# Optimization experiments

Measured on AMD Instinct MI355X. Metric: run time of the kernel, lower is better.

## Reference

```python
import jax, jax.numpy as jnp
import numpy as np

B, C, K, F = 16, 64, 128, 6
HORIZON_S = 3.0  # conflict_horizon_s default
EPS = 1e-06


def setup_inputs() -> dict:
    rng = np.random.default_rng(0)
    # base adjacency: sparse random directed graph, zero diagonal
    A = (rng.random((B, K, K)) < 0.05).astype(np.float32)
    A[:, np.arange(K), np.arange(K)] = 0.0
    # candidates: exactly one unordered-pair edit (state in {0:none,1:i->j,2:j->i})
    cand = np.repeat(A[:, None], C, axis=1).copy()
    i = rng.integers(0, K - 1, (B, C))
    j = i + 1 + (rng.integers(0, K - 1, (B, C)) % (K - 1 - i))
    state = rng.integers(0, 3, (B, C))
    bidx = np.arange(B)[:, None] * np.ones((1, C), dtype=np.int64)
    cidx = np.ones((B, 1), dtype=np.int64) * np.arange(C)[None, :]
    cand[bidx, cidx, i, j] = (state == 1).astype(np.float32)
    cand[bidx, cidx, j, i] = (state == 2).astype(np.float32)
    cand[:, 0] = A  # candidate 0 is NOOP (keep A_t)
    # agent features: (x, y, yaw, vx, vy, pad)
    feat = rng.normal(size=(B, K, F)).astype(np.float32)
    feat[..., 0:2] *= 20.0  # spread positions over ~40m
    mask = (rng.random((B, K)) > 0.1).astype(np.float32)
    return {
        "A_t": jnp.asarray(A),
        "candidate_A": jnp.asarray(cand),
        "agent_feat": jnp.asarray(feat),
        "agent_mask": jnp.asarray(mask),
    }


def _edit_tokens(A_t, candidate_A):
    # vectorized version of EBSTM.extract_edit_tokens
    Bn, Cn, Kn, _ = candidate_A.shape
    base = A_t > 0.5                      # [B,K,K]
    cb = candidate_A > 0.5                # [B,C,K,K]
    diff = cb != base[:, None]            # [B,C,K,K]
    upper = jnp.triu(jnp.ones((Kn, Kn), dtype=bool), k=1)
    pairdiff = (diff | jnp.swapaxes(diff, -1, -2)) & upper
    flat = pairdiff.reshape(Bn, Cn, Kn * Kn)
    changed = flat.any(-1)                # [B,C]
    idx = jnp.argmax(flat, axis=-1)       # first changed pair in row-major (i,j) order
    i = idx // Kn
    j = idx % Kn
    barange = jnp.arange(Bn)[:, None]
    carange = jnp.arange(Cn)[None, :]
    b_ij = base[barange, i, j]
    b_ji = base[barange, j, i]
    c_ij = cb[barange, carange, i, j]
    c_ji = cb[barange, carange, j, i]
    prev = jnp.where(b_ij & ~b_ji, 1, jnp.where(b_ji & ~b_ij, 2, 0))
    nxt = jnp.where(c_ij & ~c_ji, 1, jnp.where(c_ji & ~c_ij, 2, 0))
    tokens = jnp.stack([i, j, prev, nxt], axis=-1).astype(jnp.int32)
    return tokens * changed[..., None].astype(jnp.int32)


def _relation_state3(cb):
    # cb: bool [B,C,K,K]
    at = jnp.swapaxes(cb, -1, -2)
    return ((cb & ~at).astype(jnp.int32) * 1
            + (~cb & at).astype(jnp.int32) * 2
            + (cb & at).astype(jnp.int32) * 3)


def _batched_acyclic(cb, agent_mask):
    # vectorized Kahn zero-indegree peel, matching EBSTM._is_acyclic semantics:
    #  - indegree counts edges from ALL sources (valid or not)
    #  - only valid nodes are ever removed
    #  - special case: <=1 valid node is acyclic
    Bn, Cn, Kn, _ = cb.shape
    valid = (agent_mask > 0.5)[:, None, :]           # [B,1,K]
    Ai = cb.astype(jnp.int32)                        # [B,C,K,K]
    indeg = Ai.sum(axis=-2) * valid.astype(jnp.int32)  # [B,C,K]
    removed = jnp.zeros((Bn, Cn, Kn), dtype=bool)

    def body(t, carry):
        indeg, removed = carry
        rem = valid & (~removed) & (indeg == 0)
        dec = jnp.einsum('bci,bcij->bcj', rem.astype(jnp.int32), Ai)
        return indeg - dec, removed | rem

    indeg, removed = jax.lax.fori_loop(0, Kn, body, (indeg, removed))
    vcount = valid.astype(jnp.int32).sum(-1)          # [B,1]
    return (removed.astype(jnp.int32).sum(-1) == vcount) | (vcount <= 1)


def _pair_dists(agent_feat):
    pos = agent_feat[..., 0:2]
    vel = agent_feat[..., 3:5]
    # _pair_distance: d[b,i,j] = |pos_i - pos_j|
    d = jnp.linalg.norm(pos[:, :, None] - pos[:, None, :], axis=-1)
    # _pair_closest_approach_distance: r[b,i,j] = pos_j - pos_i
    r = pos[:, None, :] - pos[:, :, None]
    v = vel[:, None, :] - vel[:, :, None]
    vv = (v * v).sum(-1)
    rv = (r * v).sum(-1)
    t_star = jnp.clip(-rv / (vv + EPS), 0.0, HORIZON_S)
    dmin = jnp.linalg.norm(r + v * t_star[..., None], axis=-1)
    eye = jnp.eye(dmin.shape[-1], dtype=bool)[None]
    dmin = jnp.where(eye, jnp.inf, dmin)
    return jnp.stack([d, dmin], axis=0)  # [2,B,K,K]


def reference(A_t, candidate_A, agent_feat, agent_mask):
    cb = candidate_A > 0.5
    tokens = _edit_tokens(A_t, candidate_A)          # [B,C,4] int32
    rel = _relation_state3(cb)                       # [B,C,K,K] int32
    acyclic = _batched_acyclic(cb, agent_mask)       # [B,C] bool
    dists = _pair_dists(agent_feat)                  # [2,B,K,K] float32
    return tokens, rel, acyclic, dists
```

## Files before the change

kernel.cpp:

```cpp
#include <hip/hip_runtime.h>
#include <cstdint>
#include <math.h>

#define KN 128
#define BATCH 16
#define CAND 64

typedef float vfloat4 __attribute__((ext_vector_type(4)));

static constexpr size_t TOK_OFF = 0;
static constexpr size_t REL_OFF = (size_t)BATCH * CAND * 4;
static constexpr size_t ACY_OFF = REL_OFF + (size_t)BATCH * CAND * KN * KN;
static constexpr size_t DST_OFF = ACY_OFF + (size_t)BATCH * CAND;

#define DIAG_BIG 1.0e30f

__global__ __launch_bounds__(256) void prep_kernel(const float* __restrict__ A_t,
                                                   const float* __restrict__ feat,
                                                   uint32_t* __restrict__ bits,
                                                   float* __restrict__ out) {
    int t = threadIdx.x;
    {
        int tid  = blockIdx.x * 256 + t;
        int wave = tid >> 6;
        int lane = tid & 63;
        int half = wave & 1;
        int row  = wave >> 1;
        float v = A_t[(size_t)row * KN + half * 64 + lane];
        unsigned long long m = __ballot(v > 0.5f);
        if (lane == 0) {
            bits[row * 4 + half * 2]     = (uint32_t)m;
            bits[row * 4 + half * 2 + 1] = (uint32_t)(m >> 32);
        }
    }
    {
        int bi = 2 * blockIdx.x + (t >> 7);
        int b2 = bi >> 7, i = bi & 127, j = t & 127;
        const float* fi = feat + (size_t)bi * 6;
        const float* fj = feat + (size_t)(b2 * KN + j) * 6;
        float pix = fi[0], piy = fi[1], vix = fi[3], viy = fi[4];
        float pjx = fj[0], pjy = fj[1], vjx = fj[3], vjy = fj[4];
        float dx = pix - pjx, dy = piy - pjy;
        float d = sqrtf(dx * dx + dy * dy);
        float rx = pjx - pix, ry = pjy - piy;
        float vx = vjx - vix, vy = vjy - viy;
        float vv = vx * vx + vy * vy;
        float rv = rx * vx + ry * vy;
        float ts = fminf(fmaxf(-rv / (vv + 1e-6f), 0.0f), 3.0f);
        float mx = rx + vx * ts, my = ry + vy * ts;
        float dmin = (i == j) ? DIAG_BIG : sqrtf(mx * mx + my * my);
        float* o = out + DST_OFF;
        __builtin_nontemporal_store(d,    o + (size_t)(b2 * KN + i) * KN + j);
        __builtin_nontemporal_store(dmin, o + (size_t)((BATCH + b2) * KN + i) * KN + j);
    }
}

__global__ __launch_bounds__(512, 8) void main_kernel(const float* __restrict__ cand,
                                                      const float* __restrict__ mask,
                                                      const uint32_t* __restrict__ baseBits,
                                                      float* __restrict__ out) {
    __shared__ uint32_t adj[KN][5];
    __shared__ uint32_t adjT[KN][6];
    __shared__ uint32_t baseB[KN][4];
    __shared__ uint32_t validW[4];
    __shared__ uint32_t remW[4];
    __shared__ uint32_t removedW[4];
    __shared__ int      minIdx;

    const int t    = threadIdx.x;
    const int lane = t & 63;
    const int wave = t >> 6;
    const int bc   = blockIdx.x;
    const int b    = bc >> 6;

    const float* cptr = cand + (size_t)bc * (KN * KN);

    float4 c[8];
    const int sub = lane & 31;
    #pragma unroll
    for (int m = 0; m < 8; ++m) {
        int r = (m * 8 + wave) * 2 + (lane >> 5);
        c[m] = ((const float4*)(cptr + (size_t)r * KN))[sub];
    }

    if (t == 0) minIdx = 0x7fffffff;
    if (t < 4)  removedW[t] = 0;

    baseB[t >> 2][t & 3] = baseBits[b * 512 + t];

    if (wave < 2) {
        float mv = mask[b * KN + wave * 64 + lane];
        unsigned long long m = __ballot(mv > 0.5f);
        if (lane == 0) {
            validW[wave * 2]     = (uint32_t)m;
            validW[wave * 2 + 1] = (uint32_t)(m >> 32);
        }
    }

    #pragma unroll
    for (int m = 0; m < 8; ++m) {
        int r = (m * 8 + wave) * 2 + (lane >> 5);
        const float4 v = c[m];
        uint32_t nib = (v.x > 0.5f ? 1u : 0u) | (v.y > 0.5f ? 2u : 0u) |
                       (v.z > 0.5f ? 4u : 0u) | (v.w > 0.5f ? 8u : 0u);
        uint32_t word = nib << (4 * (sub & 7));
        word |= __shfl_xor(word, 1);
        word |= __shfl_xor(word, 2);
        word |= __shfl_xor(word, 4);
        if ((lane & 7) == 0) adj[r][sub >> 3] = word;
    }
    __syncthreads();

    {
        const int h  = (wave >> 1) & 1;
        const int q  = wave & 1;
        const int ch = wave >> 2;
        uint32_t rw = adj[h * 64 + lane][q * 2 + ch];
        uint32_t myLo = 0, myHi = 0;
        #pragma unroll
        for (int cc = 0; cc < 32; ++cc) {
            unsigned long long m = __ballot((rw >> cc) & 1u);
            if (lane == cc) { myLo = (uint32_t)m; myHi = (uint32_t)(m >> 32); }
        }
        if (lane < 32) {
            int col = q * 64 + ch * 32 + lane;
            adjT[col][2 * h]     = myLo;
            adjT[col][2 * h + 1] = myHi;
        }
    }
    __syncthreads();

    {
        float* relp = out + REL_OFF + (size_t)bc * (KN * KN);
        #pragma unroll
        for (int m = 0; m < 8; ++m) {
            int q  = t + 512 * m;
            int i  = q >> 5;
            int j0 = (q & 31) * 4;
            int iw = j0 >> 5, sh = j0 & 31;
            uint32_t wij = adj[i][iw];
            uint32_t wti = adjT[i][iw];
            vfloat4 o;
            o.x = (float)(((wij >> (sh + 0)) & 1u) + 2u * ((wti >> (sh + 0)) & 1u));
            o.y = (float)(((wij >> (sh + 1)) & 1u) + 2u * ((wti >> (sh + 1)) & 1u));
            o.z = (float)(((wij >> (sh + 2)) & 1u) + 2u * ((wti >> (sh + 2)) & 1u));
            o.w = (float)(((wij >> (sh + 3)) & 1u) + 2u * ((wti >> (sh + 3)) & 1u));
            __builtin_nontemporal_store(o, ((vfloat4*)relp) + q);
        }
    }

    {
        int idx = t;
        int i = idx >> 2, k = idx & 3;
        uint32_t diff = adj[i][k] ^ baseB[i][k];
        if (diff) {
            int base = k * 32;
            uint32_t up, low;
            if (i < base)            { up = diff; low = 0u; }
            else if (i >= base + 31) { up = 0u; low = (i > base + 31) ? diff : (diff & 0x7fffffffu); }
            else {
                int s = i - base;
                up  = diff & (0xffffffffu << (s + 1));
                low = diff & ((1u << s) - 1u);
            }
            int c1 = 0x7fffffff, c2 = 0x7fffffff;
            if (up)  c1 = (i << 7) | (base + __builtin_ctz(up));
            if (low) { int cc2 = base + __builtin_ctz(low); c2 = (cc2 << 7) | i; }
            int cm = min(c1, c2);
            if (cm != 0x7fffffff) atomicMin(&minIdx, cm);
        }
    }

    uint32_t cT0 = 0, cT1 = 0, cT2 = 0, cT3 = 0;
    int  indeg = 0;
    bool validT = false, removed = false;
    if (t < KN) {
        cT0 = adjT[t][0]; cT1 = adjT[t][1]; cT2 = adjT[t][2]; cT3 = adjT[t][3];
        validT = (validW[t >> 5] >> (t & 31)) & 1u;
        indeg = validT ? (__popc(cT0) + __popc(cT1) + __popc(cT2) + __popc(cT3)) : 0;
    }
    __syncthreads();

    if (t == 0) {
        float* tok = out + TOK_OFF + (size_t)bc * 4;
        int mi = minIdx;
        if (mi != 0x7fffffff) {
            int i = mi >> 7, j = mi & 127;
            uint32_t b_ij = (baseB[i][j >> 5] >> (j & 31)) & 1u;
            uint32_t b_ji = (baseB[j][i >> 5] >> (i & 31)) & 1u;
            uint32_t c_ij = (adj[i][j >> 5] >> (j & 31)) & 1u;
            uint32_t c_ji = (adj[j][i >> 5] >> (i & 31)) & 1u;
            int prev = (b_ij && !b_ji) ? 1 : ((b_ji && !b_ij) ? 2 : 0);
            int nxt  = (c_ij && !c_ji) ? 1 : ((c_ji && !c_ij) ? 2 : 0);
            tok[0] = (float)i; tok[1] = (float)j; tok[2] = (float)prev; tok[3] = (float)nxt;
        } else {
            tok[0] = 0.f; tok[1] = 0.f; tok[2] = 0.f; tok[3] = 0.f;
        }
    }

    for (int it = 0; it < KN; ++it) {
        bool rem = (t < KN) && validT && !removed && (indeg == 0);
        unsigned long long m = __ballot(rem);
        if (wave < 2 && lane == 0) {
            remW[wave * 2]     = (uint32_t)m;
            remW[wave * 2 + 1] = (uint32_t)(m >> 32);
        }
        __syncthreads();
        uint32_t r0 = remW[0], r1 = remW[1], r2 = remW[2], r3 = remW[3];
        if ((r0 | r1 | r2 | r3) == 0u) break;
        if (t < 4) removedW[t] |= remW[t];
        if (t < KN) {
            indeg -= __popc(r0 & cT0) + __popc(r1 & cT1) +
                     __popc(r2 & cT2) + __popc(r3 & cT3);
            removed = removed || rem;
        }
        __syncthreads();
    }
    __syncthreads();

    if (t == 0) {
        int rc = __popc(removedW[0]) + __popc(removedW[1]) + __popc(removedW[2]) + __popc(removedW[3]);
        int vc = __popc(validW[0]) + __popc(validW[1]) + __popc(validW[2]) + __popc(validW[3]);
        out[ACY_OFF + bc] = ((rc == vc) || (vc <= 1)) ? 1.0f : 0.0f;
    }
}

extern "C" void kernel_launch(void* const* d_in, const int* in_sizes, int n_in,
                              void* d_out, int out_size, void* d_ws, size_t ws_size,
                              hipStream_t stream) {
    const float* A_t  = (const float*)d_in[0];
    const float* cand = (const float*)d_in[1];
    const float* feat = (const float*)d_in[2];
    const float* mask = (const float*)d_in[3];
    float* out = (float*)d_out;
    uint32_t* bits = (uint32_t*)d_ws;

    prep_kernel<<<1024, 256, 0, stream>>>(A_t, feat, bits, out);
    main_kernel<<<BATCH * CAND, 512, 0, stream>>>(cand, mask, bits, out);
}
```

Measured before the change: 125.5 us.

## Split bandwidth-bound streaming from serial acyclicity logic into separate kernels

Restructures the work into a streaming kernel, where each candidate is split across two 256-thread blocks that each handle a diagonal pair of 64x64 tiles, plus a separate logic kernel. The streaming kernel also absorbs the former prep work (base bits and pair distances) as extra blocks. Bitmaps and their transposes go to workspace for a lightweight logic kernel that does edit-token and acyclicity work. The aim is to give the bandwidth-bound rel write more, smaller blocks and keep it separate from the latency-bound serial Kahn loop. The cost is an extra workspace round trip and a dependency between the prep blocks and the logic kernel, which the stream ordering of the two launches handles.

```diff
diff --git a/kernel.cpp b/kernel.cpp
--- a/kernel.cpp
+++ b/kernel.cpp
@@ -13,54 +13,174 @@
 static constexpr size_t ACY_OFF = REL_OFF + (size_t)BATCH * CAND * KN * KN;
 static constexpr size_t DST_OFF = ACY_OFF + (size_t)BATCH * CAND;
 
+static constexpr size_t WS_BASE = 0;
+static constexpr size_t WS_BITS = 8192;
+
 #define DIAG_BIG 1.0e30f
 
-__global__ __launch_bounds__(256) void prep_kernel(const float* __restrict__ A_t,
-                                                   const float* __restrict__ feat,
-                                                   uint32_t* __restrict__ bits,
-                                                   float* __restrict__ out) {
-    int t = threadIdx.x;
+__global__ __launch_bounds__(256, 8) void stream_kernel(const float* __restrict__ cand,
+                                                        const float* __restrict__ A_t,
+                                                        const float* __restrict__ feat,
+                                                        uint32_t* __restrict__ ws,
+                                                        float* __restrict__ out) {
+    const int t    = threadIdx.x;
+    const int lane = t & 63;
+    const int wave = t >> 6;
+    const int blk  = blockIdx.x;
+
+    if (blk >= 2048) {
+        const int pb = blk - 2048;
+        {
+            int tid  = pb * 256 + t;
+            int wv   = tid >> 6;
+            int ln   = tid & 63;
+            int half = wv & 1;
+            int row  = wv >> 1;
+            float v = A_t[(size_t)row * KN + half * 64 + ln];
+            unsigned long long m = __ballot(v > 0.5f);
+            if (ln == 0) {
+                ws[WS_BASE + row * 4 + half * 2]     = (uint32_t)m;
+                ws[WS_BASE + row * 4 + half * 2 + 1] = (uint32_t)(m >> 32);
+            }
+        }
+        {
+            int bi = 2 * pb + (t >> 7);
+            int b2 = bi >> 7, i = bi & 127, j = t & 127;
+            const float* fi = feat + (size_t)bi * 6;
+            const float* fj = feat + (size_t)(b2 * KN + j) * 6;
+            float pix = fi[0], piy = fi[1], vix = fi[3], viy = fi[4];
+            float pjx = fj[0], pjy = fj[1], vjx = fj[3], vjy = fj[4];
+            float dx = pix - pjx, dy = piy - pjy;
+            float d = sqrtf(dx * dx + dy * dy);
+            float rx = pjx - pix, ry = pjy - piy;
+            float vx = vjx - vix, vy = vjy - viy;
+            float vv = vx * vx + vy * vy;
+            float rv = rx * vx + ry * vy;
+            float ts = fminf(fmaxf(-rv / (vv + 1e-6f), 0.0f), 3.0f);
+            float mx = rx + vx * ts, my = ry + vy * ts;
+            float dmin = (i == j) ? DIAG_BIG : sqrtf(mx * mx + my * my);
+            float* o = out + DST_OFF;
+            __builtin_nontemporal_store(d,    o + (size_t)(b2 * KN + i) * KN + j);
+            __builtin_nontemporal_store(dmin, o + (size_t)((BATCH + b2) * KN + i) * KN + j);
+        }
+        return;
+    }
+
+    const int bc = blk >> 1;
+    const int u  = blk & 1;
+    const int RA = 0,  CA = u * 64;
+    const int RB = 64, CB = 64 - u * 64;
+
+    const vfloat4* c4 = (const vfloat4*)(cand + (size_t)bc * (KN * KN));
+
+    __shared__ uint32_t bitsA[64][3], bitsB[64][3];
+    __shared__ uint32_t bitsAT[64][3], bitsBT[64][3];
+
+    const int c4i   = t & 15;
+    const int rbase = t >> 4;
+
+    vfloat4 va[4], vb[4];
+    #pragma unroll
+    for (int k = 0; k < 4; ++k) {
+        int row = k * 16 + rbase;
+        va[k] = c4[(RA + row) * 32 + (CA >> 2) + c4i];
+        vb[k] = c4[(RB + row) * 32 + (CB >> 2) + c4i];
+    }
+    #pragma unroll
+    for (int k = 0; k < 4; ++k) {
+        int row = k * 16 + rbase;
+        {
+            vfloat4 v = va[k];
+            uint32_t nib = (v.x > 0.5f ? 1u : 0u) | (v.y > 0.5f ? 2u : 0u) |
+                           (v.z > 0.5f ? 4u : 0u) | (v.w > 0.5f ? 8u : 0u);
+            uint32_t word = nib << (4 * (c4i & 7));
+            word |= __shfl_xor(word, 1);
+            word |= __shfl_xor(word, 2);
+            word |= __shfl_xor(word, 4);
+            if ((c4i & 7) == 0) bitsA[row][c4i >> 3] = word;
+        }
+        {
+            vfloat4 v = vb[k];
+            uint32_t nib = (v.x > 0.5f ? 1u : 0u) | (v.y > 0.5f ? 2u : 0u) |
+                           (v.z > 0.5f ? 4u : 0u) | (v.w > 0.5f ? 8u : 0u);
+            uint32_t word = nib << (4 * (c4i & 7));
+            word |= __shfl_xor(word, 1);
+            word |= __shfl_xor(word, 2);
+            word |= __shfl_xor(word, 4);
+            if ((c4i & 7) == 0) bitsB[row][c4i >> 3] = word;
+        }
+    }
+    __syncthreads();
+
     {
-        int tid  = blockIdx.x * 256 + t;
-        int wave = tid >> 6;
-        int lane = tid & 63;
-        int half = wave & 1;
-        int row  = wave >> 1;
-        float v = A_t[(size_t)row * KN + half * 64 + lane];
-        unsigned long long m = __ballot(v > 0.5f);
-        if (lane == 0) {
-            bits[row * 4 + half * 2]     = (uint32_t)m;
-            bits[row * 4 + half * 2 + 1] = (uint32_t)(m >> 32);
-        }
-    }
+        uint32_t (*src)[3] = (wave < 2) ? bitsA : bitsB;
+        uint32_t (*dst)[3] = (wave < 2) ? bitsAT : bitsBT;
+        const int ch = wave & 1;
+        uint32_t rw = src[lane][ch];
+        uint32_t myLo = 0, myHi = 0;
+        #pragma unroll
+        for (int cc = 0; cc < 32; ++cc) {
+            unsigned long long m = __ballot((rw >> cc) & 1u);
+            if (lane == cc) { myLo = (uint32_t)m; myHi = (uint32_t)(m >> 32); }
+        }
+        if (lane < 32) {
+            dst[ch * 32 + lane][0] = myLo;
+            dst[ch * 32 + lane][1] = myHi;
+        }
+    }
+    __syncthreads();
+
     {
-        int bi = 2 * blockIdx.x + (t >> 7);
-        int b2 = bi >> 7, i = bi & 127, j = t & 127;
-        const float* fi = feat + (size_t)bi * 6;
-        const float* fj = feat + (size_t)(b2 * KN + j) * 6;
-        float pix = fi[0], piy = fi[1], vix = fi[3], viy = fi[4];
-        float pjx = fj[0], pjy = fj[1], vjx = fj[3], vjy = fj[4];
-        float dx = pix - pjx, dy = piy - pjy;
-        float d = sqrtf(dx * dx + dy * dy);
-        float rx = pjx - pix, ry = pjy - piy;
-        float vx = vjx - vix, vy = vjy - viy;
-        float vv = vx * vx + vy * vy;
-        float rv = rx * vx + ry * vy;
-        float ts = fminf(fmaxf(-rv / (vv + 1e-6f), 0.0f), 3.0f);
-        float mx = rx + vx * ts, my = ry + vy * ts;
-        float dmin = (i == j) ? DIAG_BIG : sqrtf(mx * mx + my * my);
-        float* o = out + DST_OFF;
-        __builtin_nontemporal_store(d,    o + (size_t)(b2 * KN + i) * KN + j);
-        __builtin_nontemporal_store(dmin, o + (size_t)((BATCH + b2) * KN + i) * KN + j);
+        vfloat4* rel4 = (vfloat4*)(out + REL_OFF + (size_t)bc * (KN * KN));
+        uint32_t (*TA)[3] = (u == 0) ? bitsAT : bitsBT;
+        uint32_t (*TB)[3] = (u == 0) ? bitsBT : bitsAT;
+        #pragma unroll
+        for (int k = 0; k < 4; ++k) {
+            int row = k * 16 + rbase;
+            int j0 = c4i * 4;
+            int iw = j0 >> 5, sh = j0 & 31;
+            {
+                uint32_t wij = bitsA[row][iw];
+                uint32_t wti = TA[row][iw];
+                vfloat4 o;
+                o.x = (float)(((wij >> (sh + 0)) & 1u) + 2u * ((wti >> (sh + 0)) & 1u));
+                o.y = (float)(((wij >> (sh + 1)) & 1u) + 2u * ((wti >> (sh + 1)) & 1u));
+                o.z = (float)(((wij >> (sh + 2)) & 1u) + 2u * ((wti >> (sh + 2)) & 1u));
+                o.w = (float)(((wij >> (sh + 3)) & 1u) + 2u * ((wti >> (sh + 3)) & 1u));
+                __builtin_nontemporal_store(o, rel4 + (RA + row) * 32 + (CA >> 2) + c4i);
+            }
+            {
+                uint32_t wij = bitsB[row][iw];
+                uint32_t wti = TB[row][iw];
+                vfloat4 o;
+                o.x = (float)(((wij >> (sh + 0)) & 1u) + 2u * ((wti >> (sh + 0)) & 1u));
+                o.y = (float)(((wij >> (sh + 1)) & 1u) + 2u * ((wti >> (sh + 1)) & 1u));
+                o.z = (float)(((wij >> (sh + 2)) & 1u) + 2u * ((wti >> (sh + 2)) & 1u));
+                o.w = (float)(((wij >> (sh + 3)) & 1u) + 2u * ((wti >> (sh + 3)) & 1u));
+                __builtin_nontemporal_store(o, rel4 + (RB + row) * 32 + (CB >> 2) + c4i);
+            }
+        }
+    }
+
+    {
+        uint32_t* wb = ws + WS_BITS + (size_t)bc * 1024;
+        int tile = t >> 7;
+        int idx  = t & 127;
+        int r = idx >> 1, w = idx & 1;
+        if (tile == 0) {
+            wb[(RA + r) * 4 + (CA >> 5) + w]       = bitsA[r][w];
+            wb[512 + (CA + r) * 4 + (RA >> 5) + w] = bitsAT[r][w];
+        } else {
+            wb[(RB + r) * 4 + (CB >> 5) + w]       = bitsB[r][w];
+            wb[512 + (CB + r) * 4 + (RB >> 5) + w] = bitsBT[r][w];
+        }
     }
 }
 
-__global__ __launch_bounds__(512, 8) void main_kernel(const float* __restrict__ cand,
-                                                      const float* __restrict__ mask,
-                                                      const uint32_t* __restrict__ baseBits,
-                                                      float* __restrict__ out) {
-    __shared__ uint32_t adj[KN][5];
-    __shared__ uint32_t adjT[KN][6];
+__global__ __launch_bounds__(256) void logic_kernel(const float* __restrict__ mask,
+                                                    const uint32_t* __restrict__ ws,
+                                                    float* __restrict__ out) {
+    __shared__ uint32_t adj[KN][4];
     __shared__ uint32_t baseB[KN][4];
     __shared__ uint32_t validW[4];
     __shared__ uint32_t remW[4];
@@ -73,20 +193,22 @@
     const int bc   = blockIdx.x;
     const int b    = bc >> 6;
 
-    const float* cptr = cand + (size_t)bc * (KN * KN);
-
-    float4 c[8];
-    const int sub = lane & 31;
-    #pragma unroll
-    for (int m = 0; m < 8; ++m) {
-        int r = (m * 8 + wave) * 2 + (lane >> 5);
-        c[m] = ((const float4*)(cptr + (size_t)r * KN))[sub];
+    const uint32_t* wb = ws + WS_BITS + (size_t)bc * 1024;
+
+    uint32_t cT0 = 0, cT1 = 0, cT2 = 0, cT3 = 0;
+    if (t < KN) {
+        uint4 at = ((const uint4*)(wb + 512))[t];
+        cT0 = at.x; cT1 = at.y; cT2 = at.z; cT3 = at.w;
+        uint4 a = ((const uint4*)wb)[t];
+        adj[t][0] = a.x; adj[t][1] = a.y; adj[t][2] = a.z; adj[t][3] = a.w;
+    } else {
+        int r = t - 128;
+        uint4 bb = ((const uint4*)(ws + WS_BASE + (size_t)b * 512))[r];
+        baseB[r][0] = bb.x; baseB[r][1] = bb.y; baseB[r][2] = bb.z; baseB[r][3] = bb.w;
     }
 
     if (t == 0) minIdx = 0x7fffffff;
     if (t < 4)  removedW[t] = 0;
-
-    baseB[t >> 2][t & 3] = baseBits[b * 512 + t];
 
     if (wave < 2) {
         float mv = mask[b * KN + wave * 64 + lane];
@@ -96,61 +218,9 @@
             validW[wave * 2 + 1] = (uint32_t)(m >> 32);
         }
     }
-
-    #pragma unroll
-    for (int m = 0; m < 8; ++m) {
-        int r = (m * 8 + wave) * 2 + (lane >> 5);
-        const float4 v = c[m];
-        uint32_t nib = (v.x > 0.5f ? 1u : 0u) | (v.y > 0.5f ? 2u : 0u) |
-                       (v.z > 0.5f ? 4u : 0u) | (v.w > 0.5f ? 8u : 0u);
-        uint32_t word = nib << (4 * (sub & 7));
-        word |= __shfl_xor(word, 1);
-        word |= __shfl_xor(word, 2);
-        word |= __shfl_xor(word, 4);
-        if ((lane & 7) == 0) adj[r][sub >> 3] = word;
-    }
-    __syncthreads();
-
-    {
-        const int h  = (wave >> 1) & 1;
-        const int q  = wave & 1;
-        const int ch = wave >> 2;
-        uint32_t rw = adj[h * 64 + lane][q * 2 + ch];
-        uint32_t myLo = 0, myHi = 0;
-        #pragma unroll
-        for (int cc = 0; cc < 32; ++cc) {
-            unsigned long long m = __ballot((rw >> cc) & 1u);
-            if (lane == cc) { myLo = (uint32_t)m; myHi = (uint32_t)(m >> 32); }
-        }
-        if (lane < 32) {
-            int col = q * 64 + ch * 32 + lane;
-            adjT[col][2 * h]     = myLo;
-            adjT[col][2 * h + 1] = myHi;
-        }
-    }
-    __syncthreads();
-
-    {
-        float* relp = out + REL_OFF + (size_t)bc * (KN * KN);
-        #pragma unroll
-        for (int m = 0; m < 8; ++m) {
-            int q  = t + 512 * m;
-            int i  = q >> 5;
-            int j0 = (q & 31) * 4;
-            int iw = j0 >> 5, sh = j0 & 31;
-            uint32_t wij = adj[i][iw];
-            uint32_t wti = adjT[i][iw];
-            vfloat4 o;
-            o.x = (float)(((wij >> (sh + 0)) & 1u) + 2u * ((wti >> (sh + 0)) & 1u));
-            o.y = (float)(((wij >> (sh + 1)) & 1u) + 2u * ((wti >> (sh + 1)) & 1u));
-            o.z = (float)(((wij >> (sh + 2)) & 1u) + 2u * ((wti >> (sh + 2)) & 1u));
-            o.w = (float)(((wij >> (sh + 3)) & 1u) + 2u * ((wti >> (sh + 3)) & 1u));
-            __builtin_nontemporal_store(o, ((vfloat4*)relp) + q);
-        }
-    }
-
-    {
-        int idx = t;
+    __syncthreads();
+
+    for (int idx = t; idx < 512; idx += 256) {
         int i = idx >> 2, k = idx & 3;
         uint32_t diff = adj[i][k] ^ baseB[i][k];
         if (diff) {
@@ -171,11 +241,9 @@
         }
     }
 
-    uint32_t cT0 = 0, cT1 = 0, cT2 = 0, cT3 = 0;
     int  indeg = 0;
     bool validT = false, removed = false;
     if (t < KN) {
-        cT0 = adjT[t][0]; cT1 = adjT[t][1]; cT2 = adjT[t][2]; cT3 = adjT[t][3];
         validT = (validW[t >> 5] >> (t & 31)) & 1u;
         indeg = validT ? (__popc(cT0) + __popc(cT1) + __popc(cT2) + __popc(cT3)) : 0;
     }
@@ -233,8 +301,8 @@
     const float* feat = (const float*)d_in[2];
     const float* mask = (const float*)d_in[3];
     float* out = (float*)d_out;
-    uint32_t* bits = (uint32_t*)d_ws;
-
-    prep_kernel<<<1024, 256, 0, stream>>>(A_t, feat, bits, out);
-    main_kernel<<<BATCH * CAND, 512, 0, stream>>>(cand, mask, bits, out);
+    uint32_t* ws = (uint32_t*)d_ws;
+
+    stream_kernel<<<3072, 256, 0, stream>>>(cand, A_t, feat, ws, out);
+    logic_kernel<<<BATCH * CAND, 256, 0, stream>>>(mask, ws, out);
 }
```

Measured after the change: 127.4 us. No clear change (+1.5%).
